# Kernel tuning notes

Hardware: AMD Instinct MI355X
Metric: run time of the kernel (lower is better)

Reference implementation:

```python
import jax, jax.numpy as jnp
import numpy as np
import math

B, S, H, D = 2, 2048, 4, 64
W1 = 64  # window size for k1/v1
W2 = 64  # window size for k2/v2
SCALE = 1.0 / math.sqrt(D)
K2_BIAS = 0.0
V2_BIAS = 0.0


def setup_inputs() -> dict:
    key = jax.random.key(0)
    ks = jax.random.split(key, 5)
    mk = lambda k: jax.random.normal(k, (B, S, H, D), dtype=jnp.float32)
    return {
        "q": mk(ks[0]),
        "k1": mk(ks[1]),
        "k2": mk(ks[2]),
        "v1": mk(ks[3]),
        "v2": mk(ks[4]),
    }


def _window_gather(x, w):
    # x: [B,S,H,D] -> [B,S,w+1,H,D] of positions i-w..i (clamped), plus validity mask [S,w+1]
    S_ = x.shape[1]
    idx = jnp.arange(S_)[:, None] + jnp.arange(-w, 1)[None, :]  # [S, w+1]
    mask = idx >= 0
    idx_c = jnp.clip(idx, 0, S_ - 1)
    return x[:, idx_c], mask


def reference(q, k1, k2, v1, v2):
    k2 = k2 + K2_BIAS
    v2 = v2 + V2_BIAS

    k1w, m1 = _window_gather(k1, W1)  # [B,S,A,H,D], [S,A]
    v1w, _ = _window_gather(v1, W1)
    k2w, m2 = _window_gather(k2, W2)  # [B,S,C,H,D], [S,C]
    v2w, _ = _window_gather(v2, W2)

    # score[b,s,h,a,c] = sum_d q[b,s,h,d]*k1w[b,s,a,h,d]*k2w[b,s,c,h,d] * SCALE
    p = q[:, :, None] * k1w  # [B,S,A,H,D]
    scores = jnp.einsum('bsahd,bschd->bshac', p, k2w) * SCALE

    mask = (m1[None, :, None, :, None] & m2[None, :, None, None, :])  # [1,S,1,A,C]
    w = jnp.where(mask, jnp.exp(scores), 0.0)  # faithful: raw exp, no max-subtract

    denom = jnp.sum(w, axis=(-2, -1)) + 1e-8  # [B,S,H]
    # numerator: sum_{a,c} w[a,c] * v1[a] * v2[c] = sum_a v1[a] * (sum_c w[a,c] v2[c])
    tmp = jnp.einsum('bshac,bschd->bsahd', w, v2w)
    num = jnp.einsum('bsahd,bsahd->bshd', tmp, v1w)
    return num / denom[..., None]
```

## Files before the change

### kernel.cpp

```cpp
#include <hip/hip_runtime.h>
#include <hip/hip_bf16.h>
#include <math.h>

#define B_ 2
#define S_ 2048
#define H_ 4
#define D_ 64
#define W_ 64
#define ST 4
#define VSTR 104
#define L2T 2144
#define EXPC 0.18033688011112042f

typedef __attribute__((ext_vector_type(8))) short short8;
typedef __attribute__((ext_vector_type(4))) unsigned short ushort4_t;
typedef __attribute__((ext_vector_type(4))) float f32x4;

__device__ __forceinline__ unsigned short cbf(float f) {
    __hip_bfloat16 h = __float2bfloat16(f);
    unsigned short u;
    __builtin_memcpy(&u, &h, 2);
    return u;
}

__global__ __launch_bounds__(256)
void cvt2_kernel(const float* __restrict__ a, const float* __restrict__ b,
                 unsigned short* __restrict__ oa, unsigned short* __restrict__ ob, int n8) {
    int i = blockIdx.x * 256 + threadIdx.x;
    if (i >= 2 * n8) return;
    const float* s = (i < n8) ? a : b;
    unsigned short* d = (i < n8) ? oa : ob;
    int k = (i < n8) ? i : i - n8;
    float4 x = ((const float4*)s)[2 * k];
    float4 y = ((const float4*)s)[2 * k + 1];
    short8 o;
    o[0]=cbf(x.x); o[1]=cbf(x.y); o[2]=cbf(x.z); o[3]=cbf(x.w);
    o[4]=cbf(y.x); o[5]=cbf(y.y); o[6]=cbf(y.z); o[7]=cbf(y.w);
    *(short8*)(d + 8 * (size_t)k) = o;
}

__global__ __launch_bounds__(256)
void v2t_kernel(const float* __restrict__ v2, unsigned short* __restrict__ v2t) {
    const int s0 = blockIdx.x * 64;
    const int h = blockIdx.y, b = blockIdx.z;
    const int tid = threadIdx.x;
    __shared__ unsigned short t[64][72];
    const size_t base_bh = (size_t)(b * S_ * H_ + h) * D_;
    const int d = tid & 63;
    for (int i = tid >> 6; i < 64; i += 4)
        t[d][i] = cbf(v2[base_bh + (size_t)(s0 + i) * (H_ * D_) + d]);
    __syncthreads();
    const size_t obase = ((size_t)(b * H_ + h) * D_) * L2T;
    const short8 z = {0,0,0,0,0,0,0,0};
    for (int idx = tid; idx < 64 * 8; idx += 256) {
        int dd = idx >> 3, c8 = idx & 7;
        *(short8*)(v2t + obase + (size_t)dd * L2T + 64 + s0 + c8 * 8) = *(short8*)&t[dd][c8 * 8];
        if (blockIdx.x == 0)
            *(short8*)(v2t + obase + (size_t)dd * L2T + c8 * 8) = z;
    }
    if (blockIdx.x == (S_ / 64) - 1) {
        for (int idx = tid; idx < 64 * 4; idx += 256) {
            int dd = idx >> 2, c8 = idx & 3;
            *(short8*)(v2t + obase + (size_t)dd * L2T + 64 + S_ + c8 * 8) = z;
        }
    }
}

__global__ __launch_bounds__(256, 3)
void tsattn_mfma(const float* __restrict__ q,
                 const unsigned short* __restrict__ k1b,
                 const unsigned short* __restrict__ k2b,
                 const float* __restrict__ v1,
                 const unsigned short* __restrict__ v2t,
                 float* __restrict__ out)
{
    const int s0  = blockIdx.x * ST;
    const int h   = blockIdx.y;
    const int b   = blockIdx.z;
    const int tid = threadIdx.x;
    const int lane = tid & 63;
    const int w    = tid >> 6;
    const int m16  = lane & 15;
    const int g4   = lane >> 4;

    __shared__ unsigned short v2T[D_][VSTR];
    __shared__ unsigned short Wst[ST][16][VSTR];

    const size_t base_bh = (size_t)(b * S_ * H_ + h) * D_;
#define ROW(j) (base_bh + (size_t)(j) * (H_ * D_))

    {
        const unsigned short* src = v2t + ((size_t)(b * H_ + h) * D_) * L2T + s0;
        for (int idx = tid; idx < 64 * 24; idx += 256) {
            int d = idx / 24, rc = idx % 24;
            *(ushort4_t*)&v2T[d][rc * 4] = *(const ushort4_t*)(src + (size_t)d * L2T + rc * 4);
        }
    }
    __syncthreads();

    const int s    = s0 + w;
    const int amin = (s >= W_) ? 0 : (W_ - s);
    const size_t qoff = ROW(s);

    float qf[16];
    {
        const float* qp = q + qoff + g4 * 8;
        #pragma unroll
        for (int kk = 0; kk < 2; ++kk) {
            float4 x = *(const float4*)(qp + kk * 32);
            float4 y = *(const float4*)(qp + kk * 32 + 4);
            qf[kk*8+0]=x.x; qf[kk*8+1]=x.y; qf[kk*8+2]=x.z; qf[kk*8+3]=x.w;
            qf[kk*8+4]=y.x; qf[kk*8+5]=y.y; qf[kk*8+6]=y.z; qf[kk*8+7]=y.w;
        }
    }

    short8 b1[5][2];
    #pragma unroll
    for (int cm = 0; cm < 5; ++cm) {
        int j = s - W_ + cm * 16 + m16;
        if (j < 0) j = 0; if (j > S_ - 1) j = S_ - 1;
        const unsigned short* kp = k2b + ROW(j) + g4 * 8;
        #pragma unroll
        for (int kk = 0; kk < 2; ++kk)
            b1[cm][kk] = *(const short8*)(kp + kk * 32);
    }

    short8 b2[4][3];
    #pragma unroll
    for (int dn = 0; dn < 4; ++dn)
        #pragma unroll
        for (int kk = 0; kk < 3; ++kk)
            b2[dn][kk] = *(const short8*)&v2T[dn * 16 + m16][kk * 32 + g4 * 8];

    #pragma unroll
    for (int r = 0; r < 4; ++r) {
        int row = g4 * 4 + r;
        if (m16 < w)      Wst[w][row][m16] = 0;
        if (m16 < 16 - w) Wst[w][row][80 + w + m16] = 0;
    }

    float dsum = 0.f;
    float pnum[4] = {0.f, 0.f, 0.f, 0.f};

    #pragma unroll
    for (int strip = 0; strip < 5; ++strip) {
        short8 a1[2];
        {
            int j = s - W_ + strip * 16 + m16;
            if (j < 0) j = 0; if (j > S_ - 1) j = S_ - 1;
            const unsigned short* kp = k1b + ROW(j) + g4 * 8;
            #pragma unroll
            for (int kk = 0; kk < 2; ++kk) {
                short8 kv = *(const short8*)(kp + kk * 32);
                short8 f;
                #pragma unroll
                for (int j8 = 0; j8 < 8; ++j8) {
                    float kf = __uint_as_float(((unsigned)(unsigned short)kv[j8]) << 16);
                    f[j8] = (short)cbf(kf * qf[kk * 8 + j8]);
                }
                a1[kk] = f;
            }
        }

        f32x4 acc1[5];
        #pragma unroll
        for (int cm = 0; cm < 5; ++cm) {
            acc1[cm] = (f32x4){0.f, 0.f, 0.f, 0.f};
            #pragma unroll
            for (int kk = 0; kk < 2; ++kk)
                acc1[cm] = __builtin_amdgcn_mfma_f32_16x16x32_bf16(a1[kk], b1[cm][kk], acc1[cm], 0, 0, 0);
        }

        #pragma unroll
        for (int cm = 0; cm < 5; ++cm) {
            const int c = cm * 16 + m16;
            const bool cok = (c >= amin) & (c <= W_);
            #pragma unroll
            for (int r = 0; r < 4; ++r) {
                const int a = strip * 16 + g4 * 4 + r;
                const bool valid = cok & (a >= amin) & (a <= W_);
                const float wv = valid ? exp2f(acc1[cm][r] * EXPC) : 0.f;
                dsum += wv;
                Wst[w][g4 * 4 + r][c + w] = cbf(wv);
            }
        }

        short8 a2[3];
        #pragma unroll
        for (int kk = 0; kk < 3; ++kk)
            a2[kk] = *(const short8*)&Wst[w][m16][kk * 32 + g4 * 8];

        #pragma unroll
        for (int dn = 0; dn < 4; ++dn) {
            f32x4 acc2 = (f32x4){0.f, 0.f, 0.f, 0.f};
            #pragma unroll
            for (int kk = 0; kk < 3; ++kk)
                acc2 = __builtin_amdgcn_mfma_f32_16x16x32_bf16(a2[kk], b2[dn][kk], acc2, 0, 0, 0);
            #pragma unroll
            for (int r = 0; r < 4; ++r) {
                const int a = strip * 16 + g4 * 4 + r;
                int j = s - W_ + a;
                if (j < 0) j = 0; if (j > S_ - 1) j = S_ - 1;
                pnum[dn] += acc2[r] * v1[ROW(j) + dn * 16 + m16];
            }
        }
    }

    #pragma unroll
    for (int off = 32; off >= 1; off >>= 1) dsum += __shfl_xor(dsum, off, 64);
    #pragma unroll
    for (int dn = 0; dn < 4; ++dn) {
        pnum[dn] += __shfl_xor(pnum[dn], 16, 64);
        pnum[dn] += __shfl_xor(pnum[dn], 32, 64);
    }
    if (lane < 16) {
        const float inv = 1.f / (dsum + 1e-8f);
        #pragma unroll
        for (int dn = 0; dn < 4; ++dn)
            out[qoff + dn * 16 + lane] = pnum[dn] * inv;
    }
#undef ROW
}

extern "C" void kernel_launch(void* const* d_in, const int* in_sizes, int n_in,
                              void* d_out, int out_size, void* d_ws, size_t ws_size,
                              hipStream_t stream) {
    const float* q  = (const float*)d_in[0];
    const float* k1 = (const float*)d_in[1];
    const float* k2 = (const float*)d_in[2];
    const float* v1 = (const float*)d_in[3];
    const float* v2 = (const float*)d_in[4];
    float* out = (float*)d_out;

    const size_t NE = (size_t)B_ * S_ * H_ * D_;
    unsigned short* k1b = (unsigned short*)d_ws;
    unsigned short* k2b = k1b + NE;
    unsigned short* v2t = k2b + NE;

    const int n8 = (int)(NE / 8);
    cvt2_kernel<<<(2 * n8 + 255) / 256, 256, 0, stream>>>(k1, k2, k1b, k2b, n8);
    v2t_kernel<<<dim3(S_ / 64, H_, B_), 256, 0, stream>>>(v2, v2t);

    dim3 grid(S_ / ST, H_, B_);
    tsattn_mfma<<<grid, 256, 0, stream>>>(q, k1b, k2b, v1, v2t, out);
}
```

Baseline: 219.3 us.

## Specialize interior blocks, drop k1 bf16 pre-pass, read v2T straight from global

```diff
diff --git a/kernel.cpp b/kernel.cpp
--- a/kernel.cpp
+++ b/kernel.cpp
@@ -8,13 +8,21 @@
 #define D_ 64
 #define W_ 64
 #define ST 4
-#define VSTR 104
+#define SROW (H_ * D_)
+#define WSTR 104
 #define L2T 2144
-#define EXPC 0.18033688011112042f
+#define QSC 0.18033688011112042f
 
 typedef __attribute__((ext_vector_type(8))) short short8;
-typedef __attribute__((ext_vector_type(4))) unsigned short ushort4_t;
 typedef __attribute__((ext_vector_type(4))) float f32x4;
+typedef __attribute__((ext_vector_type(2))) unsigned int u32x2;
+typedef __attribute__((ext_vector_type(4))) unsigned int u32x4;
+
+__device__ __forceinline__ unsigned pkbf(float lo, float hi) {
+    unsigned r;
+    asm("v_cvt_pk_bf16_f32 %0, %1, %2" : "=v"(r) : "v"(lo), "v"(hi));
+    return r;
+}
 
 __device__ __forceinline__ unsigned short cbf(float f) {
     __hip_bfloat16 h = __float2bfloat16(f);
@@ -24,19 +32,13 @@
 }
 
 __global__ __launch_bounds__(256)
-void cvt2_kernel(const float* __restrict__ a, const float* __restrict__ b,
-                 unsigned short* __restrict__ oa, unsigned short* __restrict__ ob, int n8) {
+void cvt_k2(const float* __restrict__ in, unsigned short* __restrict__ outp, int n8) {
     int i = blockIdx.x * 256 + threadIdx.x;
-    if (i >= 2 * n8) return;
-    const float* s = (i < n8) ? a : b;
-    unsigned short* d = (i < n8) ? oa : ob;
-    int k = (i < n8) ? i : i - n8;
-    float4 x = ((const float4*)s)[2 * k];
-    float4 y = ((const float4*)s)[2 * k + 1];
-    short8 o;
-    o[0]=cbf(x.x); o[1]=cbf(x.y); o[2]=cbf(x.z); o[3]=cbf(x.w);
-    o[4]=cbf(y.x); o[5]=cbf(y.y); o[6]=cbf(y.z); o[7]=cbf(y.w);
-    *(short8*)(d + 8 * (size_t)k) = o;
+    if (i >= n8) return;
+    float4 x = ((const float4*)in)[2 * i];
+    float4 y = ((const float4*)in)[2 * i + 1];
+    u32x4 o = { pkbf(x.x, x.y), pkbf(x.z, x.w), pkbf(y.x, y.y), pkbf(y.z, y.w) };
+    *(u32x4*)(outp + 8 * (size_t)i) = o;
 }
 
 __global__ __launch_bounds__(256)
@@ -48,7 +50,7 @@
     const size_t base_bh = (size_t)(b * S_ * H_ + h) * D_;
     const int d = tid & 63;
     for (int i = tid >> 6; i < 64; i += 4)
-        t[d][i] = cbf(v2[base_bh + (size_t)(s0 + i) * (H_ * D_) + d]);
+        t[d][i] = cbf(v2[base_bh + (size_t)(s0 + i) * SROW + d]);
     __syncthreads();
     const size_t obase = ((size_t)(b * H_ + h) * D_) * L2T;
     const short8 z = {0,0,0,0,0,0,0,0};
@@ -66,129 +68,108 @@
     }
 }
 
-__global__ __launch_bounds__(256, 3)
-void tsattn_mfma(const float* __restrict__ q,
-                 const unsigned short* __restrict__ k1b,
-                 const unsigned short* __restrict__ k2b,
-                 const float* __restrict__ v1,
-                 const unsigned short* __restrict__ v2t,
-                 float* __restrict__ out)
+template<bool EDGE>
+__device__ __forceinline__ void tsbody(
+    const float* __restrict__ q, const float* __restrict__ k1,
+    const unsigned short* __restrict__ k2b, const float* __restrict__ v1,
+    const unsigned short* __restrict__ v2t, float* __restrict__ out,
+    unsigned short (*Wst)[WSTR],
+    int s, int base_bh, int v2base, int m16, int g4, int lane)
 {
-    const int s0  = blockIdx.x * ST;
-    const int h   = blockIdx.y;
-    const int b   = blockIdx.z;
-    const int tid = threadIdx.x;
-    const int lane = tid & 63;
-    const int w    = tid >> 6;
-    const int m16  = lane & 15;
-    const int g4   = lane >> 4;
-
-    __shared__ unsigned short v2T[D_][VSTR];
-    __shared__ unsigned short Wst[ST][16][VSTR];
-
-    const size_t base_bh = (size_t)(b * S_ * H_ + h) * D_;
-#define ROW(j) (base_bh + (size_t)(j) * (H_ * D_))
-
-    {
-        const unsigned short* src = v2t + ((size_t)(b * H_ + h) * D_) * L2T + s0;
-        for (int idx = tid; idx < 64 * 24; idx += 256) {
-            int d = idx / 24, rc = idx % 24;
-            *(ushort4_t*)&v2T[d][rc * 4] = *(const ushort4_t*)(src + (size_t)d * L2T + rc * 4);
-        }
-    }
-    __syncthreads();
-
-    const int s    = s0 + w;
-    const int amin = (s >= W_) ? 0 : (W_ - s);
-    const size_t qoff = ROW(s);
+    const int amin = (EDGE && s < W_) ? (W_ - s) : 0;
 
     float qf[16];
     {
-        const float* qp = q + qoff + g4 * 8;
+        const float* qp = q + base_bh + s * SROW + g4 * 8;
         #pragma unroll
         for (int kk = 0; kk < 2; ++kk) {
             float4 x = *(const float4*)(qp + kk * 32);
             float4 y = *(const float4*)(qp + kk * 32 + 4);
-            qf[kk*8+0]=x.x; qf[kk*8+1]=x.y; qf[kk*8+2]=x.z; qf[kk*8+3]=x.w;
-            qf[kk*8+4]=y.x; qf[kk*8+5]=y.y; qf[kk*8+6]=y.z; qf[kk*8+7]=y.w;
+            qf[kk*8+0]=x.x*QSC; qf[kk*8+1]=x.y*QSC; qf[kk*8+2]=x.z*QSC; qf[kk*8+3]=x.w*QSC;
+            qf[kk*8+4]=y.x*QSC; qf[kk*8+5]=y.y*QSC; qf[kk*8+6]=y.z*QSC; qf[kk*8+7]=y.w*QSC;
         }
     }
 
     short8 b1[5][2];
     #pragma unroll
-    for (int cm = 0; cm < 5; ++cm) {
-        int j = s - W_ + cm * 16 + m16;
-        if (j < 0) j = 0; if (j > S_ - 1) j = S_ - 1;
-        const unsigned short* kp = k2b + ROW(j) + g4 * 8;
-        #pragma unroll
-        for (int kk = 0; kk < 2; ++kk)
-            b1[cm][kk] = *(const short8*)(kp + kk * 32);
+    for (int cs = 0; cs < 5; ++cs) {
+        int j = s - W_ + cs * 16 + m16;
+        if (EDGE) j = j < 0 ? 0 : (j > S_ - 1 ? S_ - 1 : j);
+        const unsigned short* kp = k2b + base_bh + j * SROW + g4 * 8;
+        b1[cs][0] = *(const short8*)kp;
+        b1[cs][1] = *(const short8*)(kp + 32);
     }
 
     short8 b2[4][3];
     #pragma unroll
-    for (int dn = 0; dn < 4; ++dn)
+    for (int dn = 0; dn < 4; ++dn) {
+        const unsigned short* vp = v2t + v2base + (dn * 16 + m16) * L2T + s;
         #pragma unroll
         for (int kk = 0; kk < 3; ++kk)
-            b2[dn][kk] = *(const short8*)&v2T[dn * 16 + m16][kk * 32 + g4 * 8];
-
-    #pragma unroll
-    for (int r = 0; r < 4; ++r) {
-        int row = g4 * 4 + r;
-        if (m16 < w)      Wst[w][row][m16] = 0;
-        if (m16 < 16 - w) Wst[w][row][80 + w + m16] = 0;
-    }
+            b2[dn][kk] = *(const short8*)(vp + kk * 32 + g4 * 8);
+    }
+
+    *(u32x2*)&Wst[m16][80 + g4 * 4] = (u32x2){0u, 0u};
 
     float dsum = 0.f;
     float pnum[4] = {0.f, 0.f, 0.f, 0.f};
+
+    const float* k1p0 = k1 + base_bh + (s - W_ + m16) * SROW + g4 * 8;
+    const float* v1p0 = v1 + base_bh + (s - W_ + g4 * 4) * SROW + m16;
 
     #pragma unroll
     for (int strip = 0; strip < 5; ++strip) {
         short8 a1[2];
         {
-            int j = s - W_ + strip * 16 + m16;
-            if (j < 0) j = 0; if (j > S_ - 1) j = S_ - 1;
-            const unsigned short* kp = k1b + ROW(j) + g4 * 8;
+            const float* kp;
+            if (EDGE) {
+                int j = s - W_ + strip * 16 + m16;
+                j = j < 0 ? 0 : (j > S_ - 1 ? S_ - 1 : j);
+                kp = k1 + base_bh + j * SROW + g4 * 8;
+            } else {
+                kp = k1p0 + strip * 16 * SROW;
+            }
             #pragma unroll
             for (int kk = 0; kk < 2; ++kk) {
-                short8 kv = *(const short8*)(kp + kk * 32);
-                short8 f;
-                #pragma unroll
-                for (int j8 = 0; j8 < 8; ++j8) {
-                    float kf = __uint_as_float(((unsigned)(unsigned short)kv[j8]) << 16);
-                    f[j8] = (short)cbf(kf * qf[kk * 8 + j8]);
-                }
-                a1[kk] = f;
+                float4 x = *(const float4*)(kp + kk * 32);
+                float4 y = *(const float4*)(kp + kk * 32 + 4);
+                u32x4 o = { pkbf(x.x * qf[kk*8+0], x.y * qf[kk*8+1]),
+                            pkbf(x.z * qf[kk*8+2], x.w * qf[kk*8+3]),
+                            pkbf(y.x * qf[kk*8+4], y.y * qf[kk*8+5]),
+                            pkbf(y.z * qf[kk*8+6], y.w * qf[kk*8+7]) };
+                a1[kk] = *(short8*)&o;
             }
         }
 
         f32x4 acc1[5];
         #pragma unroll
-        for (int cm = 0; cm < 5; ++cm) {
-            acc1[cm] = (f32x4){0.f, 0.f, 0.f, 0.f};
+        for (int cs = 0; cs < 5; ++cs) {
+            acc1[cs] = (f32x4){0.f, 0.f, 0.f, 0.f};
             #pragma unroll
             for (int kk = 0; kk < 2; ++kk)
-                acc1[cm] = __builtin_amdgcn_mfma_f32_16x16x32_bf16(a1[kk], b1[cm][kk], acc1[cm], 0, 0, 0);
-        }
-
-        #pragma unroll
-        for (int cm = 0; cm < 5; ++cm) {
-            const int c = cm * 16 + m16;
-            const bool cok = (c >= amin) & (c <= W_);
+                acc1[cs] = __builtin_amdgcn_mfma_f32_16x16x32_bf16(b1[cs][kk], a1[kk], acc1[cs], 0, 0, 0);
+        }
+
+        const int abs_a = strip * 16 + m16;
+        const bool aok = EDGE ? (abs_a >= amin && abs_a <= W_) : (abs_a <= W_);
+        #pragma unroll
+        for (int cs = 0; cs < 5; ++cs) {
+            float e[4];
             #pragma unroll
             for (int r = 0; r < 4; ++r) {
-                const int a = strip * 16 + g4 * 4 + r;
-                const bool valid = cok & (a >= amin) & (a <= W_);
-                const float wv = valid ? exp2f(acc1[cm][r] * EXPC) : 0.f;
+                const int c = cs * 16 + g4 * 4 + r;
+                const bool ok = aok && (c <= W_) && (!EDGE || c >= amin);
+                const float wv = ok ? __builtin_amdgcn_exp2f(acc1[cs][r]) : 0.f;
                 dsum += wv;
-                Wst[w][g4 * 4 + r][c + w] = cbf(wv);
-            }
+                e[r] = wv;
+            }
+            *(u32x2*)&Wst[m16][cs * 16 + g4 * 4] = (u32x2){ pkbf(e[0], e[1]), pkbf(e[2], e[3]) };
         }
 
         short8 a2[3];
         #pragma unroll
         for (int kk = 0; kk < 3; ++kk)
-            a2[kk] = *(const short8*)&Wst[w][m16][kk * 32 + g4 * 8];
+            a2[kk] = *(const short8*)&Wst[m16][kk * 32 + g4 * 8];
 
         #pragma unroll
         for (int dn = 0; dn < 4; ++dn) {
@@ -198,10 +179,15 @@
                 acc2 = __builtin_amdgcn_mfma_f32_16x16x32_bf16(a2[kk], b2[dn][kk], acc2, 0, 0, 0);
             #pragma unroll
             for (int r = 0; r < 4; ++r) {
-                const int a = strip * 16 + g4 * 4 + r;
-                int j = s - W_ + a;
-                if (j < 0) j = 0; if (j > S_ - 1) j = S_ - 1;
-                pnum[dn] += acc2[r] * v1[ROW(j) + dn * 16 + m16];
+                float v1v;
+                if (EDGE) {
+                    int j = s - W_ + strip * 16 + g4 * 4 + r;
+                    j = j < 0 ? 0 : (j > S_ - 1 ? S_ - 1 : j);
+                    v1v = v1[base_bh + j * SROW + dn * 16 + m16];
+                } else {
+                    v1v = v1p0[strip * 16 * SROW + r * SROW + dn * 16];
+                }
+                pnum[dn] += acc2[r] * v1v;
             }
         }
     }
@@ -217,9 +203,28 @@
         const float inv = 1.f / (dsum + 1e-8f);
         #pragma unroll
         for (int dn = 0; dn < 4; ++dn)
-            out[qoff + dn * 16 + lane] = pnum[dn] * inv;
-    }
-#undef ROW
+            out[base_bh + s * SROW + dn * 16 + lane] = pnum[dn] * inv;
+    }
+}
+
+__global__ __launch_bounds__(256, 3)
+void tsattn_mfma(const float* __restrict__ q, const float* __restrict__ k1,
+                 const unsigned short* __restrict__ k2b, const float* __restrict__ v1,
+                 const unsigned short* __restrict__ v2t, float* __restrict__ out)
+{
+    __shared__ unsigned short Wst[ST][16][WSTR];
+    const int s0 = blockIdx.x * ST;
+    const int h = blockIdx.y, b = blockIdx.z;
+    const int tid = threadIdx.x, lane = tid & 63, w = tid >> 6;
+    const int m16 = lane & 15, g4 = lane >> 4;
+    const int s = s0 + w;
+    const int base_bh = b * S_ * SROW + h * D_;
+    const int v2base = ((b * H_ + h) * D_) * L2T;
+    const bool edge = (s0 < W_) || (s0 + 18 > S_ - 1);
+    if (edge)
+        tsbody<true >(q, k1, k2b, v1, v2t, out, Wst[w], s, base_bh, v2base, m16, g4, lane);
+    else
+        tsbody<false>(q, k1, k2b, v1, v2t, out, Wst[w], s, base_bh, v2base, m16, g4, lane);
 }
 
 extern "C" void kernel_launch(void* const* d_in, const int* in_sizes, int n_in,
@@ -233,14 +238,12 @@
     float* out = (float*)d_out;
 
     const size_t NE = (size_t)B_ * S_ * H_ * D_;
-    unsigned short* k1b = (unsigned short*)d_ws;
-    unsigned short* k2b = k1b + NE;
+    unsigned short* k2b = (unsigned short*)d_ws;
     unsigned short* v2t = k2b + NE;
 
     const int n8 = (int)(NE / 8);
-    cvt2_kernel<<<(2 * n8 + 255) / 256, 256, 0, stream>>>(k1, k2, k1b, k2b, n8);
+    cvt_k2<<<(n8 + 255) / 256, 256, 0, stream>>>(k2, k2b, n8);
     v2t_kernel<<<dim3(S_ / 64, H_, B_), 256, 0, stream>>>(v2, v2t);
 
-    dim3 grid(S_ / ST, H_, B_);
-    tsattn_mfma<<<grid, 256, 0, stream>>>(q, k1b, k2b, v1, v2t, out);
-}
+    tsattn_mfma<<<dim3(S_ / ST, H_, B_), 256, 0, stream>>>(q, k1, k2b, v1, v2t, out);
+}
```

Measured after the change: 307.8 us. 1.4x slower.
